# Performance work log

Measured on AMD Instinct MI355X. Metric: run time of the kernel, lower is better.

Reference implementation:

```python
import jax, jax.numpy as jnp
import numpy as np

B, S, D, H = 4, 2048, 1024, 16
HD = D // H  # 64


def setup_inputs() -> dict:
    key = jax.random.key(0)
    k1, k2, k3 = jax.random.split(key, 3)
    return {
        "hidden_states": jax.random.normal(k1, (B, S, D), dtype=jnp.float32),
        "c_attn_w": jax.random.normal(k2, (D, 3 * D), dtype=jnp.float32) * 0.02,
        "c_attn_b": jnp.zeros((3 * D,), dtype=jnp.float32),
        "c_proj_w": jax.random.normal(k3, (D, D), dtype=jnp.float32) * 0.02,
        "c_proj_b": jnp.zeros((D,), dtype=jnp.float32),
    }


def reference(hidden_states, c_attn_w, c_attn_b, c_proj_w, c_proj_b):
    b, s, d = hidden_states.shape
    qkv = hidden_states @ c_attn_w + c_attn_b  # [B,S,3D]
    q, k, v = jnp.split(qkv, 3, axis=-1)
    # split heads -> [B,H,S,hd]
    def heads(x):
        return x.reshape(b, s, H, HD).transpose(0, 2, 1, 3)
    q, k, v = heads(q), heads(k), heads(v)
    scale = 1.0 / jnp.float32(HD) ** 0.5  # scale_attn_weights=True, no layer-idx scaling
    # fp32 scores (module forces float via autocast(False))
    w = jnp.einsum("bhqd,bhkd->bhqk", q.astype(jnp.float32), k.astype(jnp.float32)) * scale
    causal = jnp.tril(jnp.ones((s, s), dtype=bool))  # [S,S]
    mask_value = jnp.finfo(w.dtype).min
    w = jnp.where(causal[None, None], w, mask_value)
    w = jax.nn.softmax(w, axis=-1).astype(v.dtype)
    a = jnp.einsum("bhqk,bhkd->bhqd", w, v)  # [B,H,S,hd]
    a = a.transpose(0, 2, 1, 3).reshape(b, s, d)  # merge heads
    return a @ c_proj_w + c_proj_b
```

## Files before the change

### kernel.cpp

```cpp
#include <hip/hip_runtime.h>
#include <stdint.h>

typedef __bf16 bf16x8 __attribute__((ext_vector_type(8)));
typedef short s16x8 __attribute__((ext_vector_type(8)));
typedef float f32x4 __attribute__((ext_vector_type(4)));

__device__ __forceinline__ short f2bf(float f) {
  union { __bf16 h; short s; } u;
  u.h = (__bf16)f;
  return u.s;
}

__device__ __forceinline__ void async_copy16(short* lds, const short* g) {
  __builtin_amdgcn_global_load_lds((const __attribute__((address_space(1))) void*)g,
                                   (__attribute__((address_space(3))) void*)lds,
                                   16, 0, 0);
}

__global__ __launch_bounds__(256) void cast_bf16_kernel(const float* __restrict__ in,
                                                        short* __restrict__ out) {
  int i = blockIdx.x * 256 + threadIdx.x;
  float4 v = reinterpret_cast<const float4*>(in)[i];
  short4 o;
  o.x = f2bf(v.x); o.y = f2bf(v.y); o.z = f2bf(v.z); o.w = f2bf(v.w);
  reinterpret_cast<short4*>(out)[i] = o;
}

__global__ __launch_bounds__(256) void transpose_cast_kernel(const float* __restrict__ in,
                                                             short* __restrict__ out,
                                                             int R, int C) {
  __shared__ float tile[32][33];
  int c0 = blockIdx.x * 32, r0 = blockIdx.y * 32;
  int tc = threadIdx.x & 31, tr = threadIdx.x >> 5;
#pragma unroll
  for (int p = 0; p < 4; ++p)
    tile[tr + p * 8][tc] = in[(size_t)(r0 + tr + p * 8) * C + c0 + tc];
  __syncthreads();
#pragma unroll
  for (int p = 0; p < 4; ++p)
    out[(size_t)(c0 + tr + p * 8) * R + r0 + tc] = f2bf(tile[tc][tr + p * 8]);
}

template <bool OBF, bool QSCALE>
__global__ __launch_bounds__(256) void gemm128_kernel(const short* __restrict__ A,
                                                      const short* __restrict__ Bt,
                                                      const float* __restrict__ bias,
                                                      void* __restrict__ Cout,
                                                      int K, int ldc) {
  __shared__ short Asm[128 * 32];
  __shared__ short Bsm[128 * 32];
  const int tid = threadIdx.x;
  const int lane = tid & 63, wid = tid >> 6;
  const int m0 = blockIdx.y * 128, n0 = blockIdx.x * 128;
  const int wm = wid >> 1, wn = wid & 1;
  const int lr = lane & 15, lg = lane >> 4;

  f32x4 acc[4][4] = {};

  const int s1 = tid, s2 = 256 + tid;
  const short* a1 = A + (size_t)(m0 + (s1 >> 2)) * K + (s1 & 3) * 8;
  const short* a2 = A + (size_t)(m0 + (s2 >> 2)) * K + (s2 & 3) * 8;
  const short* b1 = Bt + (size_t)(n0 + (s1 >> 2)) * K + (s1 & 3) * 8;
  const short* b2 = Bt + (size_t)(n0 + (s2 >> 2)) * K + (s2 & 3) * 8;

  for (int k0 = 0; k0 < K; k0 += 32) {
    __syncthreads();
    async_copy16(&Asm[s1 * 8], a1 + k0);
    async_copy16(&Asm[s2 * 8], a2 + k0);
    async_copy16(&Bsm[s1 * 8], b1 + k0);
    async_copy16(&Bsm[s2 * 8], b2 + k0);
    __syncthreads();

    bf16x8 af[4], bf[4];
#pragma unroll
    for (int mi = 0; mi < 4; ++mi)
      af[mi] = *(const bf16x8*)&Asm[(wm * 64 + mi * 16 + lr) * 32 + lg * 8];
#pragma unroll
    for (int ni = 0; ni < 4; ++ni)
      bf[ni] = *(const bf16x8*)&Bsm[(wn * 64 + ni * 16 + lr) * 32 + lg * 8];
    __builtin_amdgcn_s_setprio(1);
#pragma unroll
    for (int mi = 0; mi < 4; ++mi)
#pragma unroll
      for (int ni = 0; ni < 4; ++ni)
        acc[mi][ni] = __builtin_amdgcn_mfma_f32_16x16x32_bf16(af[mi], bf[ni], acc[mi][ni], 0, 0, 0);
    __builtin_amdgcn_s_setprio(0);
  }

#pragma unroll
  for (int ni = 0; ni < 4; ++ni) {
    const int col = n0 + wn * 64 + ni * 16 + lr;
    const float bv = bias[col];
    const float scale = (QSCALE && col < 1024) ? 0.18033688f : 1.0f;
#pragma unroll
    for (int mi = 0; mi < 4; ++mi) {
      const int row = m0 + wm * 64 + mi * 16 + lg * 4;
#pragma unroll
      for (int j = 0; j < 4; ++j) {
        const float v = (acc[mi][ni][j] + bv) * scale;
        if constexpr (OBF)
          ((short*)Cout)[(size_t)(row + j) * ldc + col] = f2bf(v);
        else
          ((float*)Cout)[(size_t)(row + j) * ldc + col] = v;
      }
    }
  }
}

__global__ __launch_bounds__(256) void vtrans_kernel(const short* __restrict__ qkv,
                                                     short* __restrict__ vt) {
  __shared__ short tile[64][72];
  const int tid = threadIdx.x;
  const int s0 = blockIdx.x * 64;
  const int h = blockIdx.y, b = blockIdx.z;
  const short* src = qkv + (size_t)(b * 2048 + s0) * 3072 + 2048 + h * 64;
#pragma unroll
  for (int p = 0; p < 2; ++p) {
    const int r = (tid >> 3) + p * 32;
    const int c0 = (tid & 7) * 8;
    *(s16x8*)&tile[r][c0] = *(const s16x8*)(src + (size_t)r * 3072 + c0);
  }
  __syncthreads();
  short* dst = vt + (size_t)(b * 16 + h) * 64 * 2048;
#pragma unroll
  for (int p = 0; p < 2; ++p) {
    const int d = (tid >> 3) + p * 32;
    const int sl0 = (tid & 7) * 8;
    s16x8 v;
#pragma unroll
    for (int i = 0; i < 8; ++i) v[i] = tile[sl0 + i][d];
    *(s16x8*)(dst + (size_t)d * 2048 + s0 + sl0) = v;
  }
}

__global__ __launch_bounds__(256) void attn_kernel(const short* __restrict__ qkv,
                                                   const short* __restrict__ vt,
                                                   short* __restrict__ abuf) {
  __shared__ short P_lds[4][16][72];
  const int tid = threadIdx.x;
  const int lane = tid & 63, wid = tid >> 6;
  const int lr = lane & 15, lg = lane >> 4;

  const int g = blockIdx.x;
  const int w = ((g & 7) << 7) | (g >> 3);
  const int px = w & 15, h = (w >> 4) & 15, b = w >> 8;

  const int ldq = 3072;
  const short* Qb = qkv + (size_t)b * 2048 * ldq + h * 64;
  const short* Kb = Qb + 1024;
  const short* Vtb = vt + (size_t)(b * 16 + h) * 64 * 2048;

  for (int pp = 0; pp < 2; ++pp) {
    const int qsub = pp ? px : 31 - px;
    const int qrowA = qsub * 64 + wid * 16;

    bf16x8 qf[2];
#pragma unroll
    for (int gg = 0; gg < 2; ++gg)
      qf[gg] = *(const bf16x8*)(Qb + (size_t)(qrowA + lr) * ldq + gg * 32 + lg * 8);

    f32x4 o[4] = {};
    float mst[4], lst[4];
#pragma unroll
    for (int j = 0; j < 4; ++j) { mst[j] = -__builtin_inff(); lst[j] = 0.f; }

    const int ntiles = qsub + 1;

    bf16x8 kf[4][2];
#pragma unroll
    for (int ni = 0; ni < 4; ++ni)
#pragma unroll
      for (int gg = 0; gg < 2; ++gg)
        kf[ni][gg] = *(const bf16x8*)(Kb + (size_t)(ni * 16 + lr) * ldq + gg * 32 + lg * 8);

    for (int t = 0; t < ntiles; ++t) {
      const int kvt = t << 6;

      f32x4 s[4];
      __builtin_amdgcn_s_setprio(1);
#pragma unroll
      for (int ni = 0; ni < 4; ++ni) {
        f32x4 z = {0.f, 0.f, 0.f, 0.f};
        s[ni] = z;
#pragma unroll
        for (int gg = 0; gg < 2; ++gg)
          s[ni] = __builtin_amdgcn_mfma_f32_16x16x32_bf16(qf[gg], kf[ni][gg], s[ni], 0, 0, 0);
      }
      __builtin_amdgcn_s_setprio(0);

      bf16x8 kn[4][2];
      if (t + 1 < ntiles) {
        const int kvn = kvt + 64;
#pragma unroll
        for (int ni = 0; ni < 4; ++ni)
#pragma unroll
          for (int gg = 0; gg < 2; ++gg)
            kn[ni][gg] = *(const bf16x8*)(Kb + (size_t)(kvn + ni * 16 + lr) * ldq + gg * 32 + lg * 8);
      }
      bf16x8 vb[4][2];
#pragma unroll
      for (int db = 0; db < 4; ++db)
#pragma unroll
        for (int gg = 0; gg < 2; ++gg)
          vb[db][gg] = *(const bf16x8*)(Vtb + (size_t)(db * 16 + lr) * 2048 + kvt + gg * 32 + lg * 8);

      if (kvt + 63 > qrowA) {
#pragma unroll
        for (int ni = 0; ni < 4; ++ni)
#pragma unroll
          for (int j = 0; j < 4; ++j) {
            const int q = qrowA + lg * 4 + j;
            const int kv = kvt + ni * 16 + lr;
            if (kv > q) s[ni][j] = -__builtin_inff();
          }
      }

      float v4[4];
#pragma unroll
      for (int j = 0; j < 4; ++j) {
        float v = fmaxf(fmaxf(s[0][j], s[1][j]), fmaxf(s[2][j], s[3][j]));
        v = fmaxf(v, __shfl_xor(v, 1, 64));
        v = fmaxf(v, __shfl_xor(v, 2, 64));
        v = fmaxf(v, __shfl_xor(v, 4, 64));
        v = fmaxf(v, __shfl_xor(v, 8, 64));
        v4[j] = v;
      }
      float gmax = fmaxf(fmaxf(v4[0] - mst[0], v4[1] - mst[1]),
                         fmaxf(v4[2] - mst[2], v4[3] - mst[3]));
      if (!__all(gmax <= 8.f)) {
#pragma unroll
        for (int j = 0; j < 4; ++j) {
          const float mn = fmaxf(mst[j], v4[j]);
          const float alpha = exp2f(mst[j] - mn);
          mst[j] = mn;
          lst[j] *= alpha;
#pragma unroll
          for (int db = 0; db < 4; ++db)
            o[db][j] *= alpha;
        }
      }

      float psum[4] = {};
#pragma unroll
      for (int ni = 0; ni < 4; ++ni)
#pragma unroll
        for (int j = 0; j < 4; ++j) {
          const float p = exp2f(s[ni][j] - mst[j]);
          psum[j] += p;
          P_lds[wid][lg * 4 + j][ni * 16 + lr] = f2bf(p);
        }
#pragma unroll
      for (int j = 0; j < 4; ++j) {
        float v = psum[j];
        v += __shfl_xor(v, 1, 64);
        v += __shfl_xor(v, 2, 64);
        v += __shfl_xor(v, 4, 64);
        v += __shfl_xor(v, 8, 64);
        lst[j] += v;
      }

      bf16x8 pa[2];
#pragma unroll
      for (int gg = 0; gg < 2; ++gg)
        pa[gg] = *(const bf16x8*)&P_lds[wid][lr][gg * 32 + lg * 8];

      __builtin_amdgcn_s_setprio(1);
#pragma unroll
      for (int db = 0; db < 4; ++db)
#pragma unroll
        for (int gg = 0; gg < 2; ++gg)
          o[db] = __builtin_amdgcn_mfma_f32_16x16x32_bf16(pa[gg], vb[db][gg], o[db], 0, 0, 0);
      __builtin_amdgcn_s_setprio(0);

#pragma unroll
      for (int ni = 0; ni < 4; ++ni)
#pragma unroll
        for (int gg = 0; gg < 2; ++gg)
          kf[ni][gg] = kn[ni][gg];
    }

    float rl[4];
#pragma unroll
    for (int j = 0; j < 4; ++j) rl[j] = 1.0f / lst[j];
#pragma unroll
    for (int db = 0; db < 4; ++db) {
      const int col = h * 64 + db * 16 + lr;
#pragma unroll
      for (int j = 0; j < 4; ++j) {
        const int row = b * 2048 + qrowA + lg * 4 + j;
        abuf[(size_t)row * 1024 + col] = f2bf(o[db][j] * rl[j]);
      }
    }
  }
}

extern "C" void kernel_launch(void* const* d_in, const int* in_sizes, int n_in,
                              void* d_out, int out_size, void* d_ws, size_t ws_size,
                              hipStream_t stream) {
  (void)in_sizes; (void)n_in; (void)out_size; (void)ws_size;
  const float* hs = (const float*)d_in[0];
  const float* w1 = (const float*)d_in[1];
  const float* b1 = (const float*)d_in[2];
  const float* w2 = (const float*)d_in[3];
  const float* b2 = (const float*)d_in[4];

  char* w = (char*)d_ws;
  short* Xb  = (short*)(w);
  short* W1T = (short*)(w + 16777216);
  short* W2T = (short*)(w + 23068672);
  short* QKV = (short*)(w + 25165824);
  short* VT  = (short*)(w + 75497472);
  short* AB  = (short*)(w + 92274688);

  cast_bf16_kernel<<<8192, 256, 0, stream>>>(hs, Xb);
  transpose_cast_kernel<<<dim3(96, 32), 256, 0, stream>>>(w1, W1T, 1024, 3072);
  transpose_cast_kernel<<<dim3(32, 32), 256, 0, stream>>>(w2, W2T, 1024, 1024);
  gemm128_kernel<true, true><<<dim3(24, 64), 256, 0, stream>>>(Xb, W1T, b1, QKV, 1024, 3072);
  vtrans_kernel<<<dim3(32, 16, 4), 256, 0, stream>>>(QKV, VT);
  attn_kernel<<<1024, 256, 0, stream>>>(QKV, VT, AB);
  gemm128_kernel<false, false><<<dim3(8, 64), 256, 0, stream>>>(AB, W2T, b2, d_out, 1024, 1024);
}
```

Baseline: 437.6 us.

## Give each attention wave 64 query rows to reuse K/V fragments

Each wave now handles four 16-row query blocks (64 rows) instead of one, so every loaded K and V fragment feeds four times as many MFMAs. Blocks cover 256 query rows, the grid shrinks from 1024 to 256 workgroups, and waves are paired in reversed order for causal load balance. The row-sum reduction is deferred to the end and masking is applied only on the diagonal tile. In exchange, register pressure rises sharply (64 accumulator floats plus Q fragments), occupancy drops, and the smaller grid may underfill the GPU's CUs.

After: 359.1 us. -17.9%, faster.

```diff
diff --git a/kernel.cpp b/kernel.cpp
--- a/kernel.cpp
+++ b/kernel.cpp
@@ -136,14 +136,14 @@
 __global__ __launch_bounds__(256) void attn_kernel(const short* __restrict__ qkv,
                                                    const short* __restrict__ vt,
                                                    short* __restrict__ abuf) {
-  __shared__ short P_lds[4][16][72];
+  __shared__ short P_lds[4][64][72];
   const int tid = threadIdx.x;
   const int lane = tid & 63, wid = tid >> 6;
   const int lr = lane & 15, lg = lane >> 4;
 
   const int g = blockIdx.x;
-  const int w = ((g & 7) << 7) | (g >> 3);
-  const int px = w & 15, h = (w >> 4) & 15, b = w >> 8;
+  const int w = ((g & 7) << 5) | (g >> 3);
+  const int px = w & 3, h = (w >> 2) & 15, b = w >> 6;
 
   const int ldq = 3072;
   const short* Qb = qkv + (size_t)b * 2048 * ldq + h * 64;
@@ -151,20 +151,25 @@
   const short* Vtb = vt + (size_t)(b * 16 + h) * 64 * 2048;
 
   for (int pp = 0; pp < 2; ++pp) {
-    const int qsub = pp ? px : 31 - px;
-    const int qrowA = qsub * 64 + wid * 16;
-
-    bf16x8 qf[2];
-#pragma unroll
-    for (int gg = 0; gg < 2; ++gg)
-      qf[gg] = *(const bf16x8*)(Qb + (size_t)(qrowA + lr) * ldq + gg * 32 + lg * 8);
-
-    f32x4 o[4] = {};
-    float mst[4], lst[4];
-#pragma unroll
-    for (int j = 0; j < 4; ++j) { mst[j] = -__builtin_inff(); lst[j] = 0.f; }
-
-    const int ntiles = qsub + 1;
+    const int qtile = pp ? px : 7 - px;
+    const int wrow = pp ? (3 - wid) : wid;
+    const int qrowW = qtile * 256 + wrow * 64;
+
+    bf16x8 qf[4][2];
+#pragma unroll
+    for (int qb = 0; qb < 4; ++qb)
+#pragma unroll
+      for (int gg = 0; gg < 2; ++gg)
+        qf[qb][gg] = *(const bf16x8*)(Qb + (size_t)(qrowW + qb * 16 + lr) * ldq + gg * 32 + lg * 8);
+
+    f32x4 o[4][4] = {};
+    float mst[4][4], lsum[4][4];
+#pragma unroll
+    for (int qb = 0; qb < 4; ++qb)
+#pragma unroll
+      for (int j = 0; j < 4; ++j) { mst[qb][j] = -__builtin_inff(); lsum[qb][j] = 0.f; }
+
+    const int ntiles = (qrowW >> 6) + 1;
 
     bf16x8 kf[4][2];
 #pragma unroll
@@ -175,120 +180,122 @@
 
     for (int t = 0; t < ntiles; ++t) {
       const int kvt = t << 6;
-
-      f32x4 s[4];
-      __builtin_amdgcn_s_setprio(1);
-#pragma unroll
-      for (int ni = 0; ni < 4; ++ni) {
-        f32x4 z = {0.f, 0.f, 0.f, 0.f};
-        s[ni] = z;
+      const bool diag = (t == ntiles - 1);
+
+      bf16x8 vb[4][2];
+#pragma unroll
+      for (int db = 0; db < 4; ++db)
 #pragma unroll
         for (int gg = 0; gg < 2; ++gg)
-          s[ni] = __builtin_amdgcn_mfma_f32_16x16x32_bf16(qf[gg], kf[ni][gg], s[ni], 0, 0, 0);
-      }
-      __builtin_amdgcn_s_setprio(0);
-
-      bf16x8 kn[4][2];
+          vb[db][gg] = *(const bf16x8*)(Vtb + (size_t)(db * 16 + lr) * 2048 + kvt + gg * 32 + lg * 8);
+
+#pragma unroll
+      for (int qb = 0; qb < 4; ++qb) {
+        f32x4 s[4];
+        __builtin_amdgcn_s_setprio(1);
+#pragma unroll
+        for (int ni = 0; ni < 4; ++ni) {
+          f32x4 z = {0.f, 0.f, 0.f, 0.f};
+          s[ni] = z;
+#pragma unroll
+          for (int gg = 0; gg < 2; ++gg)
+            s[ni] = __builtin_amdgcn_mfma_f32_16x16x32_bf16(qf[qb][gg], kf[ni][gg], s[ni], 0, 0, 0);
+        }
+        __builtin_amdgcn_s_setprio(0);
+
+        if (diag) {
+#pragma unroll
+          for (int ni = 0; ni < 4; ++ni)
+#pragma unroll
+            for (int j = 0; j < 4; ++j) {
+              const int q = qrowW + qb * 16 + lg * 4 + j;
+              const int kv = kvt + ni * 16 + lr;
+              if (kv > q) s[ni][j] = -__builtin_inff();
+            }
+        }
+
+        float v4[4];
+#pragma unroll
+        for (int j = 0; j < 4; ++j) {
+          float v = fmaxf(fmaxf(s[0][j], s[1][j]), fmaxf(s[2][j], s[3][j]));
+          v = fmaxf(v, __shfl_xor(v, 1, 64));
+          v = fmaxf(v, __shfl_xor(v, 2, 64));
+          v = fmaxf(v, __shfl_xor(v, 4, 64));
+          v = fmaxf(v, __shfl_xor(v, 8, 64));
+          v4[j] = v;
+        }
+        const float gmax = fmaxf(fmaxf(v4[0] - mst[qb][0], v4[1] - mst[qb][1]),
+                                 fmaxf(v4[2] - mst[qb][2], v4[3] - mst[qb][3]));
+        if (!__all(gmax <= 8.f)) {
+#pragma unroll
+          for (int j = 0; j < 4; ++j) {
+            const float mn = fmaxf(mst[qb][j], v4[j]);
+            const float alpha = exp2f(mst[qb][j] - mn);
+            mst[qb][j] = mn;
+            lsum[qb][j] *= alpha;
+#pragma unroll
+            for (int db = 0; db < 4; ++db)
+              o[qb][db][j] *= alpha;
+          }
+        }
+
+#pragma unroll
+        for (int ni = 0; ni < 4; ++ni)
+#pragma unroll
+          for (int j = 0; j < 4; ++j) {
+            const float p = exp2f(s[ni][j] - mst[qb][j]);
+            lsum[qb][j] += p;
+            P_lds[wid][qb * 16 + lg * 4 + j][ni * 16 + lr] = f2bf(p);
+          }
+      }
+
       if (t + 1 < ntiles) {
         const int kvn = kvt + 64;
 #pragma unroll
         for (int ni = 0; ni < 4; ++ni)
 #pragma unroll
           for (int gg = 0; gg < 2; ++gg)
-            kn[ni][gg] = *(const bf16x8*)(Kb + (size_t)(kvn + ni * 16 + lr) * ldq + gg * 32 + lg * 8);
-      }
-      bf16x8 vb[4][2];
-#pragma unroll
-      for (int db = 0; db < 4; ++db)
+            kf[ni][gg] = *(const bf16x8*)(Kb + (size_t)(kvn + ni * 16 + lr) * ldq + gg * 32 + lg * 8);
+      }
+
+      bf16x8 pa[4][2];
+#pragma unroll
+      for (int qb = 0; qb < 4; ++qb)
 #pragma unroll
         for (int gg = 0; gg < 2; ++gg)
-          vb[db][gg] = *(const bf16x8*)(Vtb + (size_t)(db * 16 + lr) * 2048 + kvt + gg * 32 + lg * 8);
-
-      if (kvt + 63 > qrowA) {
-#pragma unroll
-        for (int ni = 0; ni < 4; ++ni)
-#pragma unroll
-          for (int j = 0; j < 4; ++j) {
-            const int q = qrowA + lg * 4 + j;
-            const int kv = kvt + ni * 16 + lr;
-            if (kv > q) s[ni][j] = -__builtin_inff();
-          }
-      }
-
-      float v4[4];
+          pa[qb][gg] = *(const bf16x8*)&P_lds[wid][qb * 16 + lr][gg * 32 + lg * 8];
+
+      __builtin_amdgcn_s_setprio(1);
+#pragma unroll
+      for (int qb = 0; qb < 4; ++qb)
+#pragma unroll
+        for (int db = 0; db < 4; ++db)
+#pragma unroll
+          for (int gg = 0; gg < 2; ++gg)
+            o[qb][db] = __builtin_amdgcn_mfma_f32_16x16x32_bf16(pa[qb][gg], vb[db][gg], o[qb][db], 0, 0, 0);
+      __builtin_amdgcn_s_setprio(0);
+    }
+
+#pragma unroll
+    for (int qb = 0; qb < 4; ++qb) {
+      float rl[4];
 #pragma unroll
       for (int j = 0; j < 4; ++j) {
-        float v = fmaxf(fmaxf(s[0][j], s[1][j]), fmaxf(s[2][j], s[3][j]));
-        v = fmaxf(v, __shfl_xor(v, 1, 64));
-        v = fmaxf(v, __shfl_xor(v, 2, 64));
-        v = fmaxf(v, __shfl_xor(v, 4, 64));
-        v = fmaxf(v, __shfl_xor(v, 8, 64));
-        v4[j] = v;
-      }
-      float gmax = fmaxf(fmaxf(v4[0] - mst[0], v4[1] - mst[1]),
-                         fmaxf(v4[2] - mst[2], v4[3] - mst[3]));
-      if (!__all(gmax <= 8.f)) {
-#pragma unroll
-        for (int j = 0; j < 4; ++j) {
-          const float mn = fmaxf(mst[j], v4[j]);
-          const float alpha = exp2f(mst[j] - mn);
-          mst[j] = mn;
-          lst[j] *= alpha;
-#pragma unroll
-          for (int db = 0; db < 4; ++db)
-            o[db][j] *= alpha;
-        }
-      }
-
-      float psum[4] = {};
-#pragma unroll
-      for (int ni = 0; ni < 4; ++ni)
-#pragma unroll
-        for (int j = 0; j < 4; ++j) {
-          const float p = exp2f(s[ni][j] - mst[j]);
-          psum[j] += p;
-          P_lds[wid][lg * 4 + j][ni * 16 + lr] = f2bf(p);
-        }
-#pragma unroll
-      for (int j = 0; j < 4; ++j) {
-        float v = psum[j];
+        float v = lsum[qb][j];
         v += __shfl_xor(v, 1, 64);
         v += __shfl_xor(v, 2, 64);
         v += __shfl_xor(v, 4, 64);
         v += __shfl_xor(v, 8, 64);
-        lst[j] += v;
-      }
-
-      bf16x8 pa[2];
-#pragma unroll
-      for (int gg = 0; gg < 2; ++gg)
-        pa[gg] = *(const bf16x8*)&P_lds[wid][lr][gg * 32 + lg * 8];
-
-      __builtin_amdgcn_s_setprio(1);
-#pragma unroll
-      for (int db = 0; db < 4; ++db)
-#pragma unroll
-        for (int gg = 0; gg < 2; ++gg)
-          o[db] = __builtin_amdgcn_mfma_f32_16x16x32_bf16(pa[gg], vb[db][gg], o[db], 0, 0, 0);
-      __builtin_amdgcn_s_setprio(0);
-
-#pragma unroll
-      for (int ni = 0; ni < 4; ++ni)
-#pragma unroll
-        for (int gg = 0; gg < 2; ++gg)
-          kf[ni][gg] = kn[ni][gg];
-    }
-
-    float rl[4];
-#pragma unroll
-    for (int j = 0; j < 4; ++j) rl[j] = 1.0f / lst[j];
-#pragma unroll
-    for (int db = 0; db < 4; ++db) {
-      const int col = h * 64 + db * 16 + lr;
-#pragma unroll
-      for (int j = 0; j < 4; ++j) {
-        const int row = b * 2048 + qrowA + lg * 4 + j;
-        abuf[(size_t)row * 1024 + col] = f2bf(o[db][j] * rl[j]);
+        rl[j] = 1.0f / v;
+      }
+#pragma unroll
+      for (int db = 0; db < 4; ++db) {
+        const int col = h * 64 + db * 16 + lr;
+#pragma unroll
+        for (int j = 0; j < 4; ++j) {
+          const int row = b * 2048 + qrowW + qb * 16 + lg * 4 + j;
+          abuf[(size_t)row * 1024 + col] = f2bf(o[qb][db][j] * rl[j]);
+        }
       }
     }
   }
@@ -317,6 +324,6 @@
   transpose_cast_kernel<<<dim3(32, 32), 256, 0, stream>>>(w2, W2T, 1024, 1024);
   gemm128_kernel<true, true><<<dim3(24, 64), 256, 0, stream>>>(Xb, W1T, b1, QKV, 1024, 3072);
   vtrans_kernel<<<dim3(32, 16, 4), 256, 0, stream>>>(QKV, VT);
-  attn_kernel<<<1024, 256, 0, stream>>>(QKV, VT, AB);
+  attn_kernel<<<256, 256, 0, stream>>>(QKV, VT, AB);
   gemm128_kernel<false, false><<<dim3(8, 64), 256, 0, stream>>>(AB, W2T, b2, d_out, 1024, 1024);
 }
```
